# Optimization experiments

Hardware: AMD Instinct MI355X
Metric: run time of the kernel (lower is better)

## Reference

```python
import jax, jax.numpy as jnp
import numpy as np

D = 1024

def setup_inputs() -> dict:
    key = jax.random.key(0)
    ks = jax.random.split(key, 7)
    s = 1.0 / np.sqrt(D)
    return {
        "x": jax.random.normal(ks[0], (4, 2048, D), dtype=jnp.float32),
        "Wq": jax.random.uniform(ks[1], (D, D), jnp.float32, -s, s),
        "bq": jax.random.uniform(ks[2], (D,), jnp.float32, -s, s),
        "Wk": jax.random.uniform(ks[3], (D, D), jnp.float32, -s, s),
        "bk": jax.random.uniform(ks[4], (D,), jnp.float32, -s, s),
        "Wv": jax.random.uniform(ks[5], (D, D), jnp.float32, -s, s),
        "bv": jax.random.uniform(ks[6], (D,), jnp.float32, -s, s),
    }

def reference(x, Wq, bq, Wk, bk, Wv, bv):
    # x: [B, S, D]
    q = jnp.einsum('bsd,de->bse', x, Wq.T) + bq
    k = jnp.einsum('bsd,de->bse', x, Wk.T) + bk
    v = jnp.einsum('bsd,de->bse', x, Wv.T) + bv
    scale = 1.0 / jnp.sqrt(jnp.float32(x.shape[-1]))
    score = jnp.einsum('bqd,bkd->bqk', q, k) * scale  # [B, S, S]
    attn = jax.nn.softmax(score, axis=-1)
    return jnp.einsum('bqk,bkd->bqd', attn, v)
```

## Files before the change

kernel.cpp:

```cpp
#include <hip/hip_runtime.h>

typedef short shortx8 __attribute__((ext_vector_type(8)));
typedef float floatx4 __attribute__((ext_vector_type(4)));
typedef unsigned short ushortx4 __attribute__((ext_vector_type(4)));
typedef unsigned short ushortx8 __attribute__((ext_vector_type(8)));

typedef __attribute__((address_space(1))) char gchar;
typedef __attribute__((address_space(3))) char lchar;

__device__ __forceinline__ void async16(const void* g, void* l) {
    __builtin_amdgcn_global_load_lds((gchar*)g, (lchar*)l, 16, 0, 0);
}

__device__ __forceinline__ unsigned short f2bf(float f) {
    union { float f; unsigned int u; } v;
    v.f = f;
    unsigned int r = v.u + 0x7fffu + ((v.u >> 16) & 1u);
    return (unsigned short)(r >> 16);
}

__device__ __forceinline__ float bf2f(unsigned short h) {
    union { unsigned int u; float f; } v;
    v.u = ((unsigned int)h) << 16;
    return v.f;
}

__device__ __forceinline__ void gemm_mainloop(const ushort* __restrict__ Arow,
                                              const ushort* __restrict__ Brow,
                                              int K, ushort* As, ushort* Bs,
                                              floatx4 acc[4][4]) {
    const int t = threadIdx.x;
    const int w = t >> 6;
    const int lane = t & 63;
    const size_t ldb = (size_t)K * 2;
    const int frs = lane >> 3;
    const int kql = (lane & 7) ^ (lane >> 4);
    const char* gA0 = (const char*)Arow + (size_t)(32 * w + frs) * ldb + (kql << 4);
    const char* gA1 = (const char*)Arow + (size_t)(32 * w + 8 + frs) * ldb + ((kql ^ 4) << 4);
    const char* gB0 = (const char*)Brow + (size_t)(32 * w + frs) * ldb + (kql << 4);
    const char* gB1 = (const char*)Brow + (size_t)(32 * w + 8 + frs) * ldb + ((kql ^ 4) << 4);
    char* lA = (char*)As + w * 4096;
    char* lB = (char*)Bs + w * 4096;
    const int ga0 = (w & 1) * 4;
    const int gb0 = (w >> 1) * 4;
    const int fr = lane & 15;
    const int kq = lane >> 4;
    const int xr = (fr >> 1) & 7;
    const int loff0 = fr * 128 + ((kq ^ xr) << 4);
    const int loff1 = fr * 128 + (((kq + 4) ^ xr) << 4);
    const int nk = K >> 6;
    for (int kt = 0; kt < nk; ++kt) {
        async16(gA0,            lA);
        async16(gA1,            lA + 1024);
        async16(gA0 + 16 * ldb, lA + 2048);
        async16(gA1 + 16 * ldb, lA + 3072);
        async16(gB0,            lB);
        async16(gB1,            lB + 1024);
        async16(gB0 + 16 * ldb, lB + 2048);
        async16(gB1 + 16 * ldb, lB + 3072);
        gA0 += 128; gA1 += 128; gB0 += 128; gB1 += 128;
        __syncthreads();
        shortx8 a0[4], b0[4], a1[4], b1[4];
#pragma unroll
        for (int i = 0; i < 4; ++i) {
            a0[i] = *(const shortx8*)((const char*)As + (ga0 + i) * 2048 + loff0);
            a1[i] = *(const shortx8*)((const char*)As + (ga0 + i) * 2048 + loff1);
        }
#pragma unroll
        for (int j = 0; j < 4; ++j) {
            b0[j] = *(const shortx8*)((const char*)Bs + (gb0 + j) * 2048 + loff0);
            b1[j] = *(const shortx8*)((const char*)Bs + (gb0 + j) * 2048 + loff1);
        }
#pragma unroll
        for (int i = 0; i < 4; ++i)
#pragma unroll
            for (int j = 0; j < 4; ++j)
                acc[i][j] = __builtin_amdgcn_mfma_f32_16x16x32_bf16(a0[i], b0[j], acc[i][j], 0, 0, 0);
#pragma unroll
        for (int i = 0; i < 4; ++i)
#pragma unroll
            for (int j = 0; j < 4; ++j)
                acc[i][j] = __builtin_amdgcn_mfma_f32_16x16x32_bf16(a1[i], b1[j], acc[i][j], 0, 0, 0);
        __syncthreads();
    }
}

__global__ __launch_bounds__(256, 3)
void qkv_gemm(const ushort* __restrict__ xb, const ushort* __restrict__ Wb,
              const float* __restrict__ bq, const float* __restrict__ bk,
              const float* __restrict__ bv,
              ushort* __restrict__ Qs, ushort* __restrict__ Ks,
              ushort* __restrict__ Vt) {
    __shared__ __align__(16) ushort lds[16384];
    const int mbase = blockIdx.y * 128;
    const int nglob = blockIdx.x * 128;
    const int z = nglob >> 10;
    const int nbase = nglob & 1023;
    floatx4 acc[4][4];
    const floatx4 zero = {0.0f, 0.0f, 0.0f, 0.0f};
#pragma unroll
    for (int i = 0; i < 4; ++i)
#pragma unroll
        for (int j = 0; j < 4; ++j) acc[i][j] = zero;

    gemm_mainloop(xb + (size_t)mbase * 1024, Wb + (size_t)nglob * 1024,
                  1024, lds, lds + 8192, acc);

    const int t = threadIdx.x, w = t >> 6, lane = t & 63;
    const int mw = (w & 1) * 64, nw = (w >> 1) * 64;
    const int r0 = mbase + mw + (lane >> 4) * 4;
    const int c0 = nbase + nw + (lane & 15);
    const float* bias = (z == 0) ? bq : (z == 1) ? bk : bv;
    const float scale = (z == 0) ? 0.03125f : 1.0f;
    float bj[4];
#pragma unroll
    for (int j = 0; j < 4; ++j) bj[j] = bias[c0 + j * 16];

    if (z < 2) {
        ushort* O = (z == 0) ? Qs : Ks;
#pragma unroll
        for (int i = 0; i < 4; ++i)
#pragma unroll
            for (int j = 0; j < 4; ++j)
#pragma unroll
                for (int r = 0; r < 4; ++r) {
                    int gr = r0 + i * 16 + r;
                    int gc = c0 + j * 16;
                    O[(size_t)gr * 1024 + gc] = f2bf((acc[i][j][r] + bj[j]) * scale);
                }
    } else {
#pragma unroll
        for (int i = 0; i < 4; ++i)
#pragma unroll
            for (int j = 0; j < 4; ++j)
#pragma unroll
                for (int r = 0; r < 4; ++r) {
                    int gr = r0 + i * 16 + r;
                    int gc = c0 + j * 16;
                    Vt[(size_t)(gr >> 11) * (1024 * 2048) + (size_t)gc * 2048 + (gr & 2047)] =
                        f2bf(acc[i][j][r] + bj[j]);
                }
    }
}

__global__ __launch_bounds__(256, 3)
void gemm_bt_bf16(const ushort* __restrict__ A, size_t sAz,
                  const ushort* __restrict__ B, size_t sBz,
                  ushort* __restrict__ C, size_t sCz, int N, int K) {
    __shared__ __align__(16) ushort lds[16384];
    const int mbase = blockIdx.y * 128;
    const int nbase = blockIdx.x * 128;
    const int z = blockIdx.z;
    floatx4 acc[4][4];
    const floatx4 zero = {0.0f, 0.0f, 0.0f, 0.0f};
#pragma unroll
    for (int i = 0; i < 4; ++i)
#pragma unroll
        for (int j = 0; j < 4; ++j) acc[i][j] = zero;

    gemm_mainloop(A + z * sAz + (size_t)mbase * K,
                  B + z * sBz + (size_t)nbase * K, K, lds, lds + 8192, acc);

    const int t = threadIdx.x, w = t >> 6, lane = t & 63;
    const int mw = (w & 1) * 64, nw = (w >> 1) * 64;
    const int r0 = mbase + mw + (lane >> 4) * 4;
    const int c0 = nbase + nw + (lane & 15);
    ushort* Cz = C + z * sCz;
#pragma unroll
    for (int i = 0; i < 4; ++i)
#pragma unroll
        for (int j = 0; j < 4; ++j)
#pragma unroll
            for (int r = 0; r < 4; ++r)
                Cz[(size_t)(r0 + i * 16 + r) * N + (c0 + j * 16)] = f2bf(acc[i][j][r]);
}

__global__ __launch_bounds__(256, 3)
void gemm_bt_f32(const ushort* __restrict__ A, size_t sAz,
                 const ushort* __restrict__ B, size_t sBz,
                 float* __restrict__ C, size_t sCz, int N, int K) {
    __shared__ __align__(16) ushort lds[16384];
    const int mbase = blockIdx.y * 128;
    const int nbase = blockIdx.x * 128;
    const int z = blockIdx.z;
    floatx4 acc[4][4];
    const floatx4 zero = {0.0f, 0.0f, 0.0f, 0.0f};
#pragma unroll
    for (int i = 0; i < 4; ++i)
#pragma unroll
        for (int j = 0; j < 4; ++j) acc[i][j] = zero;

    gemm_mainloop(A + z * sAz + (size_t)mbase * K,
                  B + z * sBz + (size_t)nbase * K, K, lds, lds + 8192, acc);

    const int t = threadIdx.x, w = t >> 6, lane = t & 63;
    const int mw = (w & 1) * 64, nw = (w >> 1) * 64;
    const int r0 = mbase + mw + (lane >> 4) * 4;
    const int c0 = nbase + nw + (lane & 15);
    float* Cz = C + z * sCz;
#pragma unroll
    for (int i = 0; i < 4; ++i)
#pragma unroll
        for (int j = 0; j < 4; ++j)
#pragma unroll
            for (int r = 0; r < 4; ++r)
                Cz[(size_t)(r0 + i * 16 + r) * N + (c0 + j * 16)] = acc[i][j][r];
}

__global__ __launch_bounds__(256)
void softmax_rows_bf16(ushort* __restrict__ SP) {
    const int row = blockIdx.x;
    ushortx8* base = (ushortx8*)(SP + (size_t)row * 2048);
    const int t = threadIdx.x;
    const int w = t >> 6, lane = t & 63;
    ushortx8 v = base[t];
    float f[8];
#pragma unroll
    for (int k = 0; k < 8; ++k) f[k] = bf2f(v[k]);
    float m = f[0];
#pragma unroll
    for (int k = 1; k < 8; ++k) m = fmaxf(m, f[k]);
    for (int o = 32; o > 0; o >>= 1) m = fmaxf(m, __shfl_down(m, o));
    __shared__ float red[4];
    if (lane == 0) red[w] = m;
    __syncthreads();
    m = fmaxf(fmaxf(red[0], red[1]), fmaxf(red[2], red[3]));

    float e[8], s = 0.0f;
#pragma unroll
    for (int k = 0; k < 8; ++k) { e[k] = __expf(f[k] - m); s += e[k]; }
    for (int o = 32; o > 0; o >>= 1) s += __shfl_down(s, o);
    __syncthreads();
    if (lane == 0) red[w] = s;
    __syncthreads();
    float inv = 1.0f / (red[0] + red[1] + red[2] + red[3]);

    ushortx8 o;
#pragma unroll
    for (int k = 0; k < 8; ++k) o[k] = f2bf(e[k] * inv);
    base[t] = o;
}

__global__ __launch_bounds__(256)
void cast_bf16_all(const float* __restrict__ x, const float* __restrict__ Wq,
                   const float* __restrict__ Wk, const float* __restrict__ Wv,
                   ushort* __restrict__ dst) {
    const int NX = 2097152;
    const int NW = 262144;
    int i = blockIdx.x * 256 + threadIdx.x;
    const float* src;
    int off;
    if (i < NX)               { src = x;  off = 0; }
    else if (i < NX + NW)     { src = Wq; off = NX; }
    else if (i < NX + 2 * NW) { src = Wk; off = NX + NW; }
    else                      { src = Wv; off = NX + 2 * NW; }
    float4 v = ((const float4*)src)[i - off];
    ushortx4 o = {f2bf(v.x), f2bf(v.y), f2bf(v.z), f2bf(v.w)};
    ((ushortx4*)dst)[i] = o;
}

extern "C" void kernel_launch(void* const* d_in, const int* in_sizes, int n_in,
                              void* d_out, int out_size, void* d_ws, size_t ws_size,
                              hipStream_t stream) {
    const float* x  = (const float*)d_in[0];
    const float* bq = (const float*)d_in[2];
    const float* bk = (const float*)d_in[4];
    const float* bv = (const float*)d_in[6];
    float* out = (float*)d_out;

    const size_t R = 8192;
    const size_t D = 1024;
    const size_t S = 2048;

    const size_t need = (4 * R * D + 3 * D * D + 4 * S * S) * 2;
    if (ws_size < need) return;

    ushort* xb = (ushort*)d_ws;
    ushort* Wb = xb + R * D;
    ushort* Qs = Wb + 3 * D * D;
    ushort* Ks = Qs + R * D;
    ushort* Vt = Ks + R * D;
    ushort* Sb = Vt + R * D;

    cast_bf16_all<<<dim3(11264), dim3(256), 0, stream>>>(
        x, (const float*)d_in[1], (const float*)d_in[3], (const float*)d_in[5], xb);

    qkv_gemm<<<dim3(24, 64), dim3(256), 0, stream>>>(xb, Wb, bq, bk, bv, Qs, Ks, Vt);

    gemm_bt_bf16<<<dim3(16, 16, 4), dim3(256), 0, stream>>>(Qs, S * D, Ks, S * D, Sb, S * S,
                                                            (int)S, (int)D);

    softmax_rows_bf16<<<dim3((unsigned)(4 * S)), dim3(256), 0, stream>>>(Sb);

    gemm_bt_f32<<<dim3(8, 16, 4), dim3(256), 0, stream>>>(Sb, S * S, Vt, D * S, out, S * D,
                                                          (int)D, (int)S);
}
```

Measured before the change: 255.7 us.

## Use 256x256 tiles with double-buffered LDS pipeline and 8-wave blocks

Replaces the 128x128 single-buffered GEMM mainloop with a 256-row tile, 512-thread version that double-buffers LDS. Async global-to-LDS loads for the next k-steps are interleaved with MFMA phases, using fine-grained barriers and wave priority hints. This aims to hide global load latency and raise data reuse per block. The cost is much larger LDS use (about one block per CU), fewer blocks in the grid, and a possible tail effect on the QKV projection.

Result: no change. 256.7 us (+0.4%).

```diff
diff --git a/kernel.cpp b/kernel.cpp
--- a/kernel.cpp
+++ b/kernel.cpp
@@ -25,91 +25,163 @@
     return v.f;
 }
 
-__device__ __forceinline__ void gemm_mainloop(const ushort* __restrict__ Arow,
-                                              const ushort* __restrict__ Brow,
-                                              int K, ushort* As, ushort* Bs,
-                                              floatx4 acc[4][4]) {
+template<int JN>
+__device__ __forceinline__ void gemm256_mainloop(
+        const ushort* __restrict__ Arow, const ushort* __restrict__ Brow,
+        int K, ushort* ldsp, floatx4 (&acc)[8][JN])
+{
     const int t = threadIdx.x;
     const int w = t >> 6;
     const int lane = t & 63;
     const size_t ldb = (size_t)K * 2;
-    const int frs = lane >> 3;
-    const int kql = (lane & 7) ^ (lane >> 4);
-    const char* gA0 = (const char*)Arow + (size_t)(32 * w + frs) * ldb + (kql << 4);
-    const char* gA1 = (const char*)Arow + (size_t)(32 * w + 8 + frs) * ldb + ((kql ^ 4) << 4);
-    const char* gB0 = (const char*)Brow + (size_t)(32 * w + frs) * ldb + (kql << 4);
-    const char* gB1 = (const char*)Brow + (size_t)(32 * w + 8 + frs) * ldb + ((kql ^ 4) << 4);
-    char* lA = (char*)As + w * 4096;
-    char* lB = (char*)Bs + w * 4096;
-    const int ga0 = (w & 1) * 4;
-    const int gb0 = (w >> 1) * 4;
-    const int fr = lane & 15;
-    const int kq = lane >> 4;
+    constexpr int ABYTES = 32768;
+    constexpr int BBYTES = JN * 8192;
+    constexpr int BUFB = ABYTES + BBYTES;
+    char* l0 = (char*)ldsp;
+    const int wst = w << 10;
+    const int sc = (((t & 7) ^ ((t >> 4) & 7)) << 4);
+    const char* gA = (const char*)Arow + (size_t)(t >> 3) * ldb + sc;
+    const char* gB = (const char*)Brow + (size_t)(t >> 3) * ldb + sc;
+    const int fr = lane & 15, kq = lane >> 4;
     const int xr = (fr >> 1) & 7;
-    const int loff0 = fr * 128 + ((kq ^ xr) << 4);
-    const int loff1 = fr * 128 + (((kq + 4) ^ xr) << 4);
+    const int ck0 = (kq ^ xr) << 4;
+    const int ck1 = ((kq + 4) ^ xr) << 4;
+    const int wm = w & 1, wn = w >> 1;
+    const int abase = (wm * 128 + fr) * 128;
+    const int bbase = (wn * (JN * 16) + fr) * 128;
+
+#define STA(buf, kt, R) async16(gA + (size_t)(R) * ldb + (size_t)(kt) * 128, \
+                                l0 + (buf) * BUFB + (R) * 128 + wst)
+#define STB(buf, kt, R) async16(gB + (size_t)(R) * ldb + (size_t)(kt) * 128, \
+                                l0 + (buf) * BUFB + ABYTES + (R) * 128 + wst)
+#define LDA4(buf, mb, ck)                                                          \
+    a0 = *(const shortx8*)(l0 + (buf) * BUFB + abase + ((mb) + 0) * 2048 + (ck));  \
+    a1 = *(const shortx8*)(l0 + (buf) * BUFB + abase + ((mb) + 1) * 2048 + (ck));  \
+    a2 = *(const shortx8*)(l0 + (buf) * BUFB + abase + ((mb) + 2) * 2048 + (ck));  \
+    a3 = *(const shortx8*)(l0 + (buf) * BUFB + abase + ((mb) + 3) * 2048 + (ck));
+#define LDBJ(buf, ck)                                                              \
+    _Pragma("unroll")                                                              \
+    for (int n = 0; n < JN; ++n)                                                   \
+        b[n] = *(const shortx8*)(l0 + (buf) * BUFB + ABYTES + bbase + n * 2048 + (ck));
+#define PHASE_MFMA(MB)                                                             \
+    __builtin_amdgcn_s_setprio(1);                                                 \
+    _Pragma("unroll")                                                              \
+    for (int n = 0; n < JN; ++n) {                                                 \
+        acc[(MB)+0][n] = __builtin_amdgcn_mfma_f32_16x16x32_bf16(a0, b[n], acc[(MB)+0][n], 0, 0, 0); \
+        acc[(MB)+1][n] = __builtin_amdgcn_mfma_f32_16x16x32_bf16(a1, b[n], acc[(MB)+1][n], 0, 0, 0); \
+        acc[(MB)+2][n] = __builtin_amdgcn_mfma_f32_16x16x32_bf16(a2, b[n], acc[(MB)+2][n], 0, 0, 0); \
+        acc[(MB)+3][n] = __builtin_amdgcn_mfma_f32_16x16x32_bf16(a3, b[n], acc[(MB)+3][n], 0, 0, 0); \
+    }                                                                              \
+    __builtin_amdgcn_s_setprio(0);
+#define BAR() __builtin_amdgcn_s_barrier()
+#define VMW()                                              \
+    asm volatile("s_waitcnt vmcnt(2)" ::: "memory");       \
+    BAR();                                                 \
+    __builtin_amdgcn_sched_barrier(0);
+
     const int nk = K >> 6;
-    for (int kt = 0; kt < nk; ++kt) {
-        async16(gA0,            lA);
-        async16(gA1,            lA + 1024);
-        async16(gA0 + 16 * ldb, lA + 2048);
-        async16(gA1 + 16 * ldb, lA + 3072);
-        async16(gB0,            lB);
-        async16(gB1,            lB + 1024);
-        async16(gB0 + 16 * ldb, lB + 2048);
-        async16(gB1 + 16 * ldb, lB + 3072);
-        gA0 += 128; gA1 += 128; gB0 += 128; gB1 += 128;
-        __syncthreads();
-        shortx8 a0[4], b0[4], a1[4], b1[4];
-#pragma unroll
-        for (int i = 0; i < 4; ++i) {
-            a0[i] = *(const shortx8*)((const char*)As + (ga0 + i) * 2048 + loff0);
-            a1[i] = *(const shortx8*)((const char*)As + (ga0 + i) * 2048 + loff1);
-        }
-#pragma unroll
-        for (int j = 0; j < 4; ++j) {
-            b0[j] = *(const shortx8*)((const char*)Bs + (gb0 + j) * 2048 + loff0);
-            b1[j] = *(const shortx8*)((const char*)Bs + (gb0 + j) * 2048 + loff1);
-        }
-#pragma unroll
-        for (int i = 0; i < 4; ++i)
-#pragma unroll
-            for (int j = 0; j < 4; ++j)
-                acc[i][j] = __builtin_amdgcn_mfma_f32_16x16x32_bf16(a0[i], b0[j], acc[i][j], 0, 0, 0);
-#pragma unroll
-        for (int i = 0; i < 4; ++i)
-#pragma unroll
-            for (int j = 0; j < 4; ++j)
-                acc[i][j] = __builtin_amdgcn_mfma_f32_16x16x32_bf16(a1[i], b1[j], acc[i][j], 0, 0, 0);
-        __syncthreads();
+    const int nit = nk >> 1;
+
+    STA(0, 0, 0); STA(0, 0, 64); STA(0, 0, 128); STA(0, 0, 192);
+    STB(0, 0, 0); STB(0, 0, 64);
+    if (JN == 4) { STB(0, 0, 128); STB(0, 0, 192); }
+    STA(1, 1, 0); STA(1, 1, 128);
+    VMW();
+
+    shortx8 a0, a1, a2, a3;
+    shortx8 b[JN];
+
+    for (int it = 0; it < nit; ++it) {
+        const int T = 2 * it;
+        int Tc2 = T + 2; if (Tc2 >= nk) Tc2 = T;
+        int Tc3 = T + 3; if (Tc3 >= nk) Tc3 = nk - 1;
+
+        LDA4(0, 0, ck0); LDBJ(0, ck0);
+        STA(1, T + 1, 64); STA(1, T + 1, 192);
+        BAR();
+        PHASE_MFMA(0);
+        BAR();
+
+        LDA4(0, 4, ck0);
+        STB(1, T + 1, 0);
+        if (JN == 4) STB(1, T + 1, 64);
+        BAR();
+        PHASE_MFMA(4);
+        BAR();
+
+        LDA4(0, 0, ck1); LDBJ(0, ck1);
+        if (JN == 4) { STB(1, T + 1, 128); STB(1, T + 1, 192); }
+        else         { STB(1, T + 1, 64); }
+        BAR();
+        PHASE_MFMA(0);
+        BAR();
+
+        LDA4(0, 4, ck1);
+        STA(0, Tc2, 0); STA(0, Tc2, 128);
+        BAR();
+        PHASE_MFMA(4);
+        VMW();
+
+        LDA4(1, 0, ck0); LDBJ(1, ck0);
+        STA(0, Tc2, 64); STA(0, Tc2, 192);
+        BAR();
+        PHASE_MFMA(0);
+        BAR();
+
+        LDA4(1, 4, ck0);
+        STB(0, Tc2, 0);
+        if (JN == 4) STB(0, Tc2, 64);
+        BAR();
+        PHASE_MFMA(4);
+        BAR();
+
+        LDA4(1, 0, ck1); LDBJ(1, ck1);
+        if (JN == 4) { STB(0, Tc2, 128); STB(0, Tc2, 192); }
+        else         { STB(0, Tc2, 64); }
+        BAR();
+        PHASE_MFMA(0);
+        BAR();
+
+        LDA4(1, 4, ck1);
+        STA(1, Tc3, 0); STA(1, Tc3, 128);
+        BAR();
+        PHASE_MFMA(4);
+        VMW();
     }
-}
-
-__global__ __launch_bounds__(256, 3)
+#undef STA
+#undef STB
+#undef LDA4
+#undef LDBJ
+#undef PHASE_MFMA
+#undef BAR
+#undef VMW
+}
+
+__global__ __launch_bounds__(512, 2)
 void qkv_gemm(const ushort* __restrict__ xb, const ushort* __restrict__ Wb,
               const float* __restrict__ bq, const float* __restrict__ bk,
               const float* __restrict__ bv,
               ushort* __restrict__ Qs, ushort* __restrict__ Ks,
               ushort* __restrict__ Vt) {
-    __shared__ __align__(16) ushort lds[16384];
-    const int mbase = blockIdx.y * 128;
-    const int nglob = blockIdx.x * 128;
+    __shared__ __align__(16) ushort lds[65536];
+    const int mbase = blockIdx.y * 256;
+    const int nglob = blockIdx.x * 256;
     const int z = nglob >> 10;
     const int nbase = nglob & 1023;
-    floatx4 acc[4][4];
+    floatx4 acc[8][4];
     const floatx4 zero = {0.0f, 0.0f, 0.0f, 0.0f};
 #pragma unroll
-    for (int i = 0; i < 4; ++i)
+    for (int i = 0; i < 8; ++i)
 #pragma unroll
         for (int j = 0; j < 4; ++j) acc[i][j] = zero;
 
-    gemm_mainloop(xb + (size_t)mbase * 1024, Wb + (size_t)nglob * 1024,
-                  1024, lds, lds + 8192, acc);
+    gemm256_mainloop<4>(xb + (size_t)mbase * 1024, Wb + (size_t)nglob * 1024,
+                        1024, lds, acc);
 
     const int t = threadIdx.x, w = t >> 6, lane = t & 63;
-    const int mw = (w & 1) * 64, nw = (w >> 1) * 64;
-    const int r0 = mbase + mw + (lane >> 4) * 4;
-    const int c0 = nbase + nw + (lane & 15);
+    const int wm = w & 1, wn = w >> 1;
+    const int r0 = mbase + wm * 128 + (lane >> 4) * 4;
+    const int c0 = nbase + wn * 64 + (lane & 15);
     const float* bias = (z == 0) ? bq : (z == 1) ? bk : bv;
     const float scale = (z == 0) ? 0.03125f : 1.0f;
     float bj[4];
@@ -117,20 +189,18 @@
     for (int j = 0; j < 4; ++j) bj[j] = bias[c0 + j * 16];
 
     if (z < 2) {
-        ushort* O = (z == 0) ? Qs : Ks;
-#pragma unroll
-        for (int i = 0; i < 4; ++i)
+        ushort* O = z ? Ks : Qs;
+#pragma unroll
+        for (int i = 0; i < 8; ++i)
 #pragma unroll
             for (int j = 0; j < 4; ++j)
 #pragma unroll
-                for (int r = 0; r < 4; ++r) {
-                    int gr = r0 + i * 16 + r;
-                    int gc = c0 + j * 16;
-                    O[(size_t)gr * 1024 + gc] = f2bf((acc[i][j][r] + bj[j]) * scale);
-                }
+                for (int r = 0; r < 4; ++r)
+                    O[(size_t)(r0 + i * 16 + r) * 1024 + (c0 + j * 16)] =
+                        f2bf((acc[i][j][r] + bj[j]) * scale);
     } else {
 #pragma unroll
-        for (int i = 0; i < 4; ++i)
+        for (int i = 0; i < 8; ++i)
 #pragma unroll
             for (int j = 0; j < 4; ++j)
 #pragma unroll
@@ -143,31 +213,31 @@
     }
 }
 
-__global__ __launch_bounds__(256, 3)
+__global__ __launch_bounds__(512, 2)
 void gemm_bt_bf16(const ushort* __restrict__ A, size_t sAz,
                   const ushort* __restrict__ B, size_t sBz,
                   ushort* __restrict__ C, size_t sCz, int N, int K) {
-    __shared__ __align__(16) ushort lds[16384];
-    const int mbase = blockIdx.y * 128;
-    const int nbase = blockIdx.x * 128;
+    __shared__ __align__(16) ushort lds[65536];
+    const int mbase = blockIdx.y * 256;
+    const int nbase = blockIdx.x * 256;
     const int z = blockIdx.z;
-    floatx4 acc[4][4];
+    floatx4 acc[8][4];
     const floatx4 zero = {0.0f, 0.0f, 0.0f, 0.0f};
 #pragma unroll
-    for (int i = 0; i < 4; ++i)
+    for (int i = 0; i < 8; ++i)
 #pragma unroll
         for (int j = 0; j < 4; ++j) acc[i][j] = zero;
 
-    gemm_mainloop(A + z * sAz + (size_t)mbase * K,
-                  B + z * sBz + (size_t)nbase * K, K, lds, lds + 8192, acc);
+    gemm256_mainloop<4>(A + z * sAz + (size_t)mbase * K,
+                        B + z * sBz + (size_t)nbase * K, K, lds, acc);
 
     const int t = threadIdx.x, w = t >> 6, lane = t & 63;
-    const int mw = (w & 1) * 64, nw = (w >> 1) * 64;
-    const int r0 = mbase + mw + (lane >> 4) * 4;
-    const int c0 = nbase + nw + (lane & 15);
+    const int wm = w & 1, wn = w >> 1;
+    const int r0 = mbase + wm * 128 + (lane >> 4) * 4;
+    const int c0 = nbase + wn * 64 + (lane & 15);
     ushort* Cz = C + z * sCz;
 #pragma unroll
-    for (int i = 0; i < 4; ++i)
+    for (int i = 0; i < 8; ++i)
 #pragma unroll
         for (int j = 0; j < 4; ++j)
 #pragma unroll
@@ -175,33 +245,33 @@
                 Cz[(size_t)(r0 + i * 16 + r) * N + (c0 + j * 16)] = f2bf(acc[i][j][r]);
 }
 
-__global__ __launch_bounds__(256, 3)
+__global__ __launch_bounds__(512, 2)
 void gemm_bt_f32(const ushort* __restrict__ A, size_t sAz,
                  const ushort* __restrict__ B, size_t sBz,
                  float* __restrict__ C, size_t sCz, int N, int K) {
-    __shared__ __align__(16) ushort lds[16384];
-    const int mbase = blockIdx.y * 128;
+    __shared__ __align__(16) ushort lds[49152];
+    const int mbase = blockIdx.y * 256;
     const int nbase = blockIdx.x * 128;
     const int z = blockIdx.z;
-    floatx4 acc[4][4];
+    floatx4 acc[8][2];
     const floatx4 zero = {0.0f, 0.0f, 0.0f, 0.0f};
 #pragma unroll
-    for (int i = 0; i < 4; ++i)
-#pragma unroll
-        for (int j = 0; j < 4; ++j) acc[i][j] = zero;
-
-    gemm_mainloop(A + z * sAz + (size_t)mbase * K,
-                  B + z * sBz + (size_t)nbase * K, K, lds, lds + 8192, acc);
+    for (int i = 0; i < 8; ++i)
+#pragma unroll
+        for (int j = 0; j < 2; ++j) acc[i][j] = zero;
+
+    gemm256_mainloop<2>(A + z * sAz + (size_t)mbase * K,
+                        B + z * sBz + (size_t)nbase * K, K, lds, acc);
 
     const int t = threadIdx.x, w = t >> 6, lane = t & 63;
-    const int mw = (w & 1) * 64, nw = (w >> 1) * 64;
-    const int r0 = mbase + mw + (lane >> 4) * 4;
-    const int c0 = nbase + nw + (lane & 15);
+    const int wm = w & 1, wn = w >> 1;
+    const int r0 = mbase + wm * 128 + (lane >> 4) * 4;
+    const int c0 = nbase + wn * 32 + (lane & 15);
     float* Cz = C + z * sCz;
 #pragma unroll
-    for (int i = 0; i < 4; ++i)
-#pragma unroll
-        for (int j = 0; j < 4; ++j)
+    for (int i = 0; i < 8; ++i)
+#pragma unroll
+        for (int j = 0; j < 2; ++j)
 #pragma unroll
             for (int r = 0; r < 4; ++r)
                 Cz[(size_t)(r0 + i * 16 + r) * N + (c0 + j * 16)] = acc[i][j][r];
@@ -285,13 +355,13 @@
     cast_bf16_all<<<dim3(11264), dim3(256), 0, stream>>>(
         x, (const float*)d_in[1], (const float*)d_in[3], (const float*)d_in[5], xb);
 
-    qkv_gemm<<<dim3(24, 64), dim3(256), 0, stream>>>(xb, Wb, bq, bk, bv, Qs, Ks, Vt);
-
-    gemm_bt_bf16<<<dim3(16, 16, 4), dim3(256), 0, stream>>>(Qs, S * D, Ks, S * D, Sb, S * S,
-                                                            (int)S, (int)D);
+    qkv_gemm<<<dim3(12, 32), dim3(512), 0, stream>>>(xb, Wb, bq, bk, bv, Qs, Ks, Vt);
+
+    gemm_bt_bf16<<<dim3(8, 8, 4), dim3(512), 0, stream>>>(Qs, S * D, Ks, S * D, Sb, S * S,
+                                                          (int)S, (int)D);
 
     softmax_rows_bf16<<<dim3((unsigned)(4 * S)), dim3(256), 0, stream>>>(Sb);
 
-    gemm_bt_f32<<<dim3(8, 16, 4), dim3(256), 0, stream>>>(Sb, S * S, Vt, D * S, out, S * D,
-                                                          (int)D, (int)S);
-}
+    gemm_bt_f32<<<dim3(8, 8, 4), dim3(512), 0, stream>>>(Sb, S * S, Vt, D * S, out, S * D,
+                                                         (int)D, (int)S);
+}
```
